# Optimization experiments

Hardware: AMD Instinct MI355X
Metric: run time of the kernel (lower is better)

The kernel has to match this reference:

```python
import jax, jax.numpy as jnp
import numpy as np

N = 100_000      # nodes
E = 1_600_000    # edges (avg degree 16)
F_IN = 128
H = 128
C = 10
G = 2000         # graphs
S = 200          # sets
MAX_SET = G // S # 10; uniform set sizes -> static max_set_size (see notes)


def _linear_init(key, fan_in, fan_out):
    s = 1.0 / np.sqrt(fan_in)
    kw, kb = jax.random.split(key)
    W = jax.random.uniform(kw, (fan_in, fan_out), minval=-s, maxval=s, dtype=jnp.float32)
    b = jax.random.uniform(kb, (fan_out,), minval=-s, maxval=s, dtype=jnp.float32)
    return W, b


def setup_inputs() -> dict:
    key = jax.random.key(0)
    ks = jax.random.split(key, 10)
    x = jax.random.normal(ks[0], (N, F_IN), dtype=jnp.float32)
    edge_index = jax.random.randint(ks[1], (2, E), 0, N, dtype=jnp.int32)
    batch = ((jnp.arange(N) * G) // N).astype(jnp.int32)          # sorted, 50 nodes/graph
    set_batch = (jnp.arange(G) % S).astype(jnp.int32)             # 10 graphs/set
    W1, b1 = _linear_init(ks[2], F_IN, H)
    W2, b2 = _linear_init(ks[3], H, H)
    W3, b3 = _linear_init(ks[4], H, H)
    psiW1, psib1 = _linear_init(ks[5], H, H)
    psiW2, psib2 = _linear_init(ks[6], H, H)
    phiW1, phib1 = _linear_init(ks[7], H, H)
    phiW2, phib2 = _linear_init(ks[8], H, C)
    return dict(x=x, edge_index=edge_index, batch=batch, set_batch=set_batch,
                W1=W1, b1=b1, W2=W2, b2=b2, W3=W3, b3=b3,
                psiW1=psiW1, psib1=psib1, psiW2=psiW2, psib2=psib2,
                phiW1=phiW1, phib1=phib1, phiW2=phiW2, phib2=phib2)


def _gcn_conv(x, src, dst, norm, W, b):
    # GCNConv: out = scatter_add(norm * (xW)[src] -> dst) + b
    h = x @ W
    msg = h[src] * norm[:, None]
    return jax.ops.segment_sum(msg, dst, num_segments=N) + b


def reference(x, edge_index, batch, set_batch,
              W1, b1, W2, b2, W3, b3,
              psiW1, psib1, psiW2, psib2, phiW1, phib1, phiW2, phib2):
    # add self loops, symmetric normalization D^-1/2 (A+I) D^-1/2
    loops = jnp.arange(N, dtype=edge_index.dtype)
    src = jnp.concatenate([edge_index[0], loops])
    dst = jnp.concatenate([edge_index[1], loops])
    deg = jax.ops.segment_sum(jnp.ones(src.shape, x.dtype), dst, num_segments=N)
    dinv = jnp.where(deg > 0, jax.lax.rsqrt(deg), 0.0)
    norm = dinv[src] * dinv[dst]

    h = jax.nn.relu(_gcn_conv(x, src, dst, norm, W1, b1))   # dropout is eval-mode identity
    h = jax.nn.relu(_gcn_conv(h, src, dst, norm, W2, b2))
    h = jax.nn.relu(_gcn_conv(h, src, dst, norm, W3, b3))

    # global mean pool over nodes -> [G, H]
    sums = jax.ops.segment_sum(h, batch, num_segments=G)
    cnts = jax.ops.segment_sum(jnp.ones((N,), h.dtype), batch, num_segments=G)
    graph_emb = sums / jnp.maximum(cnts, 1.0)[:, None]

    # ragged-to-padded pack: [S, MAX_SET, H]
    set_sizes = jax.ops.segment_sum(jnp.ones((G,), jnp.int32), set_batch, num_segments=S)
    offsets = jnp.concatenate([jnp.zeros((1,), jnp.int32), jnp.cumsum(set_sizes)])
    sorted_idx = jnp.argsort(set_batch)                      # stable by default
    positions_sorted = jnp.arange(G, dtype=jnp.int32) - offsets[set_batch[sorted_idx]]
    positions = jnp.zeros((G,), jnp.int32).at[sorted_idx].set(positions_sorted)
    x_pad = jnp.zeros((S, MAX_SET, H), x.dtype).at[set_batch, positions].set(graph_emb)

    # DeepSets: phi(sum_i psi(x_i))
    p = jnp.tanh(jax.nn.relu(x_pad @ psiW1 + psib1) @ psiW2 + psib2)
    agg = p.sum(axis=1)                                      # [S, H]
    return jax.nn.relu(agg @ phiW1 + phib1) @ phiW2 + phib2  # [S, C]
```

## Files before the change

### kernel.cpp

```cpp
#include <hip/hip_runtime.h>
#include <hip/hip_bf16.h>
#include <hip/hip_fp16.h>
#include <math.h>

#define NN 100000
#define EE 1600000
#define HH 128
#define GG 2000
#define SS 200
#define CC 10
#define NPG 50
#define PGS 10
#define NCLS 128
#define CLSW 782
#define EPB 4096
#define NBLKH 391
#define SCAN_N (NCLS * NBLKH)

typedef _Float16 f16x8 __attribute__((ext_vector_type(8)));
typedef float    f32x4 __attribute__((ext_vector_type(4)));


__global__ __launch_bounds__(256) void histo_kernel(const int* __restrict__ ei_dst,
                                                    int* __restrict__ blkcnt) {
    __shared__ int h[4][NCLS];
    for (int i = threadIdx.x; i < 4 * NCLS; i += 256) ((int*)h)[i] = 0;
    __syncthreads();
    int w = threadIdx.x >> 6;
    int base = blockIdx.x * EPB;
#pragma unroll
    for (int i = 0; i < 16; ++i) {
        int idx = base + i * 256 + threadIdx.x;
        if (idx < EE) {
            int d = __builtin_nontemporal_load(ei_dst + idx);
            atomicAdd(&h[w][(unsigned)d / CLSW], 1);
        }
    }
    __syncthreads();
    for (int c = threadIdx.x; c < NCLS; c += 256)
        blkcnt[c * NBLKH + blockIdx.x] = h[0][c] + h[1][c] + h[2][c] + h[3][c];
}

__global__ void scan_chunk_kernel(const int* __restrict__ v, int* __restrict__ outp,
                                  int* __restrict__ bsum, int n) {
    __shared__ int s[256];
    int tid = threadIdx.x;
    int i = blockIdx.x * 256 + tid;
    int x = (i < n) ? v[i] : 0;
    s[tid] = x;
    __syncthreads();
    for (int off = 1; off < 256; off <<= 1) {
        int y = (tid >= off) ? s[tid - off] : 0;
        __syncthreads();
        s[tid] += y;
        __syncthreads();
    }
    if (i < n) outp[i + 1] = s[tid];
    if (tid == 255) bsum[blockIdx.x] = s[255];
}

__global__ void scan_bsums_kernel(int* bsum, int nb) {
    __shared__ int s[512];
    int tid = threadIdx.x;
    int x = (tid < nb) ? bsum[tid] : 0;
    s[tid] = x;
    __syncthreads();
    for (int off = 1; off < 512; off <<= 1) {
        int y = (tid >= off) ? s[tid - off] : 0;
        __syncthreads();
        s[tid] += y;
        __syncthreads();
    }
    if (tid < nb) bsum[tid] = s[tid];
}

__global__ void scan_finish_kernel(int* __restrict__ outp, const int* __restrict__ bsum, int n) {
    int i = blockIdx.x * 256 + threadIdx.x;
    if (i < n) {
        if (blockIdx.x > 0) outp[i + 1] += bsum[blockIdx.x - 1];
    }
    if (i == 0) outp[0] = 0;
}

__global__ __launch_bounds__(256) void scatter_bin_kernel(const int* __restrict__ ei,
                                                          const int* __restrict__ blkoff,
                                                          long long* __restrict__ ebin) {
    __shared__ int cur[NCLS];
    for (int c = threadIdx.x; c < NCLS; c += 256) cur[c] = blkoff[c * NBLKH + blockIdx.x];
    __syncthreads();
    int base = blockIdx.x * EPB;
#pragma unroll
    for (int i = 0; i < 16; ++i) {
        int idx = base + i * 256 + threadIdx.x;
        if (idx < EE) {
            int s = __builtin_nontemporal_load(ei + idx);
            int d = __builtin_nontemporal_load(ei + EE + idx);
            int c = (unsigned)d / CLSW;
            int pos = atomicAdd(&cur[c], 1);
            ebin[pos] = ((long long)d << 32) | (unsigned)s;
        }
    }
}

__global__ __launch_bounds__(256) void count_dinv_kernel(const long long* __restrict__ ebin,
                                                         const int* __restrict__ blkoff,
                                                         int* __restrict__ degi,
                                                         float* __restrict__ dinv) {
    __shared__ int cnt[CLSW];
    int c = blockIdx.x;
    for (int i = threadIdx.x; i < CLSW; i += 256) cnt[i] = 0;
    __syncthreads();
    int beg = blkoff[c * NBLKH];
    int end = blkoff[(c + 1) * NBLKH];
    int n0 = c * CLSW;
    for (int k = beg + threadIdx.x; k < end; k += 256) {
        long long e = __builtin_nontemporal_load(ebin + k);
        atomicAdd(&cnt[(int)(e >> 32) - n0], 1);
    }
    __syncthreads();
    int nn = min(n0 + CLSW, NN) - n0;
    for (int i = threadIdx.x; i < nn; i += 256) {
        degi[n0 + i] = cnt[i];
        dinv[n0 + i] = 1.0f / sqrtf((float)(cnt[i] + 1));
    }
}

__global__ __launch_bounds__(256) void fill_class_kernel(const long long* __restrict__ ebin,
                                                         const int* __restrict__ blkoff,
                                                         const int* __restrict__ row_ptr,
                                                         int* __restrict__ col) {
    __shared__ int cur[CLSW];
    int c = blockIdx.x;
    int n0 = c * CLSW;
    int nn = min(n0 + CLSW, NN) - n0;
    for (int i = threadIdx.x; i < nn; i += 256) cur[i] = row_ptr[n0 + i];
    __syncthreads();
    int beg = blkoff[c * NBLKH];
    int end = blkoff[(c + 1) * NBLKH];
    for (int k = beg + threadIdx.x; k < end; k += 256) {
        long long e = __builtin_nontemporal_load(ebin + k);
        int s = (int)(e & 0xffffffffll);
        int d = (int)(e >> 32);
        int o = atomicAdd(&cur[d - n0], 1);
        col[o] = s;
    }
}


#define WTP 136

template <bool IN32>
__global__ __launch_bounds__(256) void gemm_mfma_kernel(const void* __restrict__ Xv,
                                                        const float* __restrict__ W,
                                                        const float* __restrict__ dinv,
                                                        _Float16* __restrict__ Y, int nrows) {
    __shared__ _Float16 Wt[128][WTP];
    __shared__ _Float16 Ob[128][WTP];
    int tid = threadIdx.x;
    int row0 = blockIdx.x * 128;

    const float4* W4 = (const float4*)W;
#pragma unroll
    for (int it = 0; it < 16; ++it) {
        int f = it * 256 + tid;
        int k = f >> 5;
        int c = (f & 31) << 2;
        float4 v = W4[f];
        Wt[c + 0][k] = (_Float16)v.x;
        Wt[c + 1][k] = (_Float16)v.y;
        Wt[c + 2][k] = (_Float16)v.z;
        Wt[c + 3][k] = (_Float16)v.w;
    }
    __syncthreads();

    int wave = tid >> 6;
    int l = tid & 63;
    int arow = l & 15;
    int kg = l >> 4;
    int baseRow = row0 + wave * 32;

    f16x8 afrag[2][4];
#pragma unroll
    for (int rt = 0; rt < 2; ++rt) {
        int r = baseRow + rt * 16 + arow;
        r = min(r, nrows - 1);
        if (IN32) {
            const float* xr = ((const float*)Xv) + (size_t)r * 128;
#pragma unroll
            for (int ks = 0; ks < 4; ++ks) {
                int k0 = ks * 32 + kg * 8;
                float4 a = ((const float4*)xr)[k0 >> 2];
                float4 b = ((const float4*)xr)[(k0 >> 2) + 1];
                f16x8 v;
                v[0] = (_Float16)a.x; v[1] = (_Float16)a.y;
                v[2] = (_Float16)a.z; v[3] = (_Float16)a.w;
                v[4] = (_Float16)b.x; v[5] = (_Float16)b.y;
                v[6] = (_Float16)b.z; v[7] = (_Float16)b.w;
                afrag[rt][ks] = v;
            }
        } else {
            const f16x8* xr = (const f16x8*)(((const _Float16*)Xv) + (size_t)r * 128);
#pragma unroll
            for (int ks = 0; ks < 4; ++ks) afrag[rt][ks] = xr[ks * 4 + kg];
        }
    }

    f32x4 acc[2][8];
#pragma unroll
    for (int rt = 0; rt < 2; ++rt)
#pragma unroll
        for (int ct = 0; ct < 8; ++ct) acc[rt][ct] = (f32x4){0.f, 0.f, 0.f, 0.f};

#pragma unroll
    for (int ct = 0; ct < 8; ++ct) {
#pragma unroll
        for (int ks = 0; ks < 4; ++ks) {
            f16x8 b = *(const f16x8*)&Wt[ct * 16 + arow][ks * 32 + kg * 8];
            acc[0][ct] = __builtin_amdgcn_mfma_f32_16x16x32_f16(afrag[0][ks], b, acc[0][ct], 0, 0, 0);
            acc[1][ct] = __builtin_amdgcn_mfma_f32_16x16x32_f16(afrag[1][ks], b, acc[1][ct], 0, 0, 0);
        }
    }

    float dv[2][4];
#pragma unroll
    for (int rt = 0; rt < 2; ++rt)
#pragma unroll
        for (int j = 0; j < 4; ++j) {
            int r = baseRow + rt * 16 + 4 * kg + j;
            dv[rt][j] = dinv[min(r, nrows - 1)];
        }

#pragma unroll
    for (int rt = 0; rt < 2; ++rt)
#pragma unroll
        for (int ct = 0; ct < 8; ++ct)
#pragma unroll
            for (int j = 0; j < 4; ++j)
                Ob[wave * 32 + rt * 16 + 4 * kg + j][ct * 16 + arow] =
                    (_Float16)(acc[rt][ct][j] * dv[rt][j]);

#pragma unroll
    for (int i = 0; i < 8; ++i) {
        int q = i * 64 + l;
        int lrow = q >> 4;
        int c = q & 15;
        int r = baseRow + lrow;
        if (r < nrows) {
            f16x8 v = *(const f16x8*)&Ob[wave * 32 + lrow][c * 8];
            *(f16x8*)(Y + (size_t)r * 128 + c * 8) = v;
        }
    }
}


__global__ __launch_bounds__(256) void aggregate_kernel(const __half* __restrict__ hw,
                                                        const int* __restrict__ rp,
                                                        const int* __restrict__ col,
                                                        const float* __restrict__ dinv,
                                                        const float* __restrict__ bias,
                                                        __half* __restrict__ outp, int n) {
    int wid = threadIdx.x >> 6;
    int lane = threadIdx.x & 63;
    int i = blockIdx.x * 4 + wid;
    if (i >= n) return;
    const __half2* hw2 = (const __half2*)hw;
    float2 a0, a1, a2, a3;
    {
        float2 self = __half22float2(hw2[(size_t)i * 64 + lane]);
        a0.x = self.x; a0.y = self.y;
    }
    a1 = make_float2(0.f, 0.f);
    a2 = make_float2(0.f, 0.f);
    a3 = make_float2(0.f, 0.f);
    int j0 = rp[i], j1 = rp[i + 1];
    int j = j0;
    for (; j + 8 <= j1; j += 8) {
        int s0 = col[j + 0];
        int s1 = col[j + 1];
        int s2 = col[j + 2];
        int s3 = col[j + 3];
        int s4 = col[j + 4];
        int s5 = col[j + 5];
        int s6 = col[j + 6];
        int s7 = col[j + 7];
        __half2 v0 = hw2[(size_t)s0 * 64 + lane];
        __half2 v1 = hw2[(size_t)s1 * 64 + lane];
        __half2 v2 = hw2[(size_t)s2 * 64 + lane];
        __half2 v3 = hw2[(size_t)s3 * 64 + lane];
        __half2 v4 = hw2[(size_t)s4 * 64 + lane];
        __half2 v5 = hw2[(size_t)s5 * 64 + lane];
        __half2 v6 = hw2[(size_t)s6 * 64 + lane];
        __half2 v7 = hw2[(size_t)s7 * 64 + lane];
        float2 f;
        f = __half22float2(v0); a0.x += f.x; a0.y += f.y;
        f = __half22float2(v1); a1.x += f.x; a1.y += f.y;
        f = __half22float2(v2); a2.x += f.x; a2.y += f.y;
        f = __half22float2(v3); a3.x += f.x; a3.y += f.y;
        f = __half22float2(v4); a0.x += f.x; a0.y += f.y;
        f = __half22float2(v5); a1.x += f.x; a1.y += f.y;
        f = __half22float2(v6); a2.x += f.x; a2.y += f.y;
        f = __half22float2(v7); a3.x += f.x; a3.y += f.y;
    }
    for (; j + 4 <= j1; j += 4) {
        int s0 = col[j + 0];
        int s1 = col[j + 1];
        int s2 = col[j + 2];
        int s3 = col[j + 3];
        __half2 v0 = hw2[(size_t)s0 * 64 + lane];
        __half2 v1 = hw2[(size_t)s1 * 64 + lane];
        __half2 v2 = hw2[(size_t)s2 * 64 + lane];
        __half2 v3 = hw2[(size_t)s3 * 64 + lane];
        float2 f;
        f = __half22float2(v0); a0.x += f.x; a0.y += f.y;
        f = __half22float2(v1); a1.x += f.x; a1.y += f.y;
        f = __half22float2(v2); a2.x += f.x; a2.y += f.y;
        f = __half22float2(v3); a3.x += f.x; a3.y += f.y;
    }
    for (; j < j1; ++j) {
        int s = col[j];
        float2 f = __half22float2(hw2[(size_t)s * 64 + lane]);
        a0.x += f.x; a0.y += f.y;
    }
    float di = dinv[i];
    float2 acc;
    acc.x = ((a0.x + a1.x) + (a2.x + a3.x)) * di;
    acc.y = ((a0.y + a1.y) + (a2.y + a3.y)) * di;
    float2 bv = ((const float2*)bias)[lane];
    float rx = fmaxf(acc.x + bv.x, 0.f);
    float ry = fmaxf(acc.y + bv.y, 0.f);
    ((__half2*)outp)[(size_t)i * 64 + lane] = __floats2half2_rn(rx, ry);
}


__global__ __launch_bounds__(256) void pool_kernel(const __half* __restrict__ h,
                                                   float* __restrict__ gemb) {
    int wid = threadIdx.x >> 6;
    int lane = threadIdx.x & 63;
    int g = blockIdx.x * 4 + wid;
    if (g >= GG) return;
    const __half2* h2 = (const __half2*)h;
    float2 acc = {0.f, 0.f};
    size_t base = (size_t)g * NPG * 64;
    for (int r = 0; r < NPG; ++r) {
        float2 v = __half22float2(h2[base + (size_t)r * 64 + lane]);
        acc.x += v.x;
        acc.y += v.y;
    }
    float2 o;
    o.x = acc.x / (float)NPG;
    o.y = acc.y / (float)NPG;
    ((float2*)gemb)[(size_t)g * 64 + lane] = o;
}


__global__ __launch_bounds__(128) void psi_kernel(const float* __restrict__ gemb,
                                                  const float* __restrict__ W1,
                                                  const float* __restrict__ b1,
                                                  const float* __restrict__ W2,
                                                  const float* __restrict__ b2,
                                                  float* __restrict__ pbuf) {
    __shared__ float e[128];
    __shared__ float t[128];
    int g = blockIdx.x;
    int c = threadIdx.x;
    e[c] = gemb[(size_t)g * 128 + c];
    __syncthreads();
    float acc = b1[c];
#pragma unroll 8
    for (int k = 0; k < 128; ++k) acc += e[k] * W1[k * 128 + c];
    t[c] = fmaxf(acc, 0.f);
    __syncthreads();
    float acc2 = b2[c];
#pragma unroll 8
    for (int k = 0; k < 128; ++k) acc2 += t[k] * W2[k * 128 + c];
    pbuf[(size_t)g * 128 + c] = tanhf(acc2);
}


__global__ __launch_bounds__(128) void phi_kernel(const float* __restrict__ pbuf,
                                                  const float* __restrict__ W1,
                                                  const float* __restrict__ b1,
                                                  const float* __restrict__ W2,
                                                  const float* __restrict__ b2,
                                                  float* __restrict__ out) {
    __shared__ float a[128];
    __shared__ float u[128];
    int s = blockIdx.x;
    int c = threadIdx.x;
    float acc = 0.f;
#pragma unroll
    for (int p = 0; p < PGS; ++p) acc += pbuf[(size_t)(s + p * SS) * 128 + c];
    a[c] = acc;
    __syncthreads();
    float acc1 = b1[c];
#pragma unroll 8
    for (int k = 0; k < 128; ++k) acc1 += a[k] * W1[k * 128 + c];
    u[c] = fmaxf(acc1, 0.f);
    __syncthreads();
    if (c < CC) {
        float acc2 = b2[c];
#pragma unroll 8
        for (int k = 0; k < 128; ++k) acc2 += u[k] * W2[k * CC + c];
        out[(size_t)s * CC + c] = acc2;
    }
}


extern "C" void kernel_launch(void* const* d_in, const int* in_sizes, int n_in,
                              void* d_out, int out_size, void* d_ws, size_t ws_size,
                              hipStream_t stream) {
    const float* x   = (const float*)d_in[0];
    const int* ei    = (const int*)d_in[1];
    const float* W1  = (const float*)d_in[4];
    const float* b1  = (const float*)d_in[5];
    const float* W2  = (const float*)d_in[6];
    const float* b2  = (const float*)d_in[7];
    const float* W3  = (const float*)d_in[8];
    const float* b3  = (const float*)d_in[9];
    const float* pW1 = (const float*)d_in[10];
    const float* pb1 = (const float*)d_in[11];
    const float* pW2 = (const float*)d_in[12];
    const float* pb2 = (const float*)d_in[13];
    const float* fW1 = (const float*)d_in[14];
    const float* fb1 = (const float*)d_in[15];
    const float* fW2 = (const float*)d_in[16];
    const float* fb2 = (const float*)d_in[17];
    float* out = (float*)d_out;

    char* p = (char*)d_ws;
    auto alloc = [&](size_t bytes) {
        char* r = p;
        p += (bytes + 255) & ~(size_t)255;
        return r;
    };
    int*       degi    = (int*)alloc((size_t)NN * 4);
    float*     dinv    = (float*)alloc((size_t)NN * 4);
    int*       row_ptr = (int*)alloc((size_t)(NN + 1) * 4);
    int*       bsum    = (int*)alloc(512 * 4);
    int*       bsum2   = (int*)alloc(512 * 4);
    int*       blkcnt  = (int*)alloc((size_t)SCAN_N * 4);
    int*       blkoff  = (int*)alloc((size_t)(SCAN_N + 1) * 4);
    int*       col     = (int*)alloc((size_t)EE * 4);
    long long* ebin    = (long long*)alloc((size_t)EE * 8);
    _Float16*  bufA    = (_Float16*)alloc((size_t)NN * HH * 2);
    __half*    bufB    = (__half*)alloc((size_t)NN * HH * 2);
    float*     gemb    = (float*)alloc((size_t)GG * HH * 4);
    float*     pbuf    = (float*)alloc((size_t)GG * HH * 4);

    const int nblkN = (NN + 255) / 256;
    const int nblkS = (SCAN_N + 255) / 256;

    histo_kernel<<<NBLKH, 256, 0, stream>>>(ei + EE, blkcnt);
    scan_chunk_kernel<<<nblkS, 256, 0, stream>>>(blkcnt, blkoff, bsum2, SCAN_N);
    scan_bsums_kernel<<<1, 512, 0, stream>>>(bsum2, nblkS);
    scan_finish_kernel<<<nblkS, 256, 0, stream>>>(blkoff, bsum2, SCAN_N);
    scatter_bin_kernel<<<NBLKH, 256, 0, stream>>>(ei, blkoff, ebin);
    count_dinv_kernel<<<NCLS, 256, 0, stream>>>(ebin, blkoff, degi, dinv);
    scan_chunk_kernel<<<nblkN, 256, 0, stream>>>(degi, row_ptr, bsum, NN);
    scan_bsums_kernel<<<1, 512, 0, stream>>>(bsum, nblkN);
    scan_finish_kernel<<<nblkN, 256, 0, stream>>>(row_ptr, bsum, NN);
    fill_class_kernel<<<NCLS, 256, 0, stream>>>(ebin, blkoff, row_ptr, col);

    const int gemmBlocks = (NN + 127) / 128;
    const int aggBlocks  = (NN + 3) / 4;

    gemm_mfma_kernel<true><<<gemmBlocks, 256, 0, stream>>>(x, W1, dinv, bufA, NN);
    aggregate_kernel<<<aggBlocks, 256, 0, stream>>>((const __half*)bufA, row_ptr, col, dinv, b1, bufB, NN);
    gemm_mfma_kernel<false><<<gemmBlocks, 256, 0, stream>>>(bufB, W2, dinv, bufA, NN);
    aggregate_kernel<<<aggBlocks, 256, 0, stream>>>((const __half*)bufA, row_ptr, col, dinv, b2, bufB, NN);
    gemm_mfma_kernel<false><<<gemmBlocks, 256, 0, stream>>>(bufB, W3, dinv, bufA, NN);
    aggregate_kernel<<<aggBlocks, 256, 0, stream>>>((const __half*)bufA, row_ptr, col, dinv, b3, bufB, NN);

    pool_kernel<<<(GG + 3) / 4, 256, 0, stream>>>(bufB, gemb);
    psi_kernel<<<GG, 128, 0, stream>>>(gemb, pW1, pb1, pW2, pb2, pbuf);
    phi_kernel<<<SS, 128, 0, stream>>>(pbuf, fW1, fb1, fW2, fb2, out);
}
```

Before: 380.6 us.

## Fuse row_ptr scan into degree count and split aggregation across half-waves

```diff
diff --git a/kernel.cpp b/kernel.cpp
--- a/kernel.cpp
+++ b/kernel.cpp
@@ -104,9 +104,10 @@
 
 __global__ __launch_bounds__(256) void count_dinv_kernel(const long long* __restrict__ ebin,
                                                          const int* __restrict__ blkoff,
-                                                         int* __restrict__ degi,
+                                                         int* __restrict__ row_ptr,
                                                          float* __restrict__ dinv) {
     __shared__ int cnt[CLSW];
+    __shared__ int part[256];
     int c = blockIdx.x;
     for (int i = threadIdx.x; i < CLSW; i += 256) cnt[i] = 0;
     __syncthreads();
@@ -119,10 +120,35 @@
     }
     __syncthreads();
     int nn = min(n0 + CLSW, NN) - n0;
-    for (int i = threadIdx.x; i < nn; i += 256) {
-        degi[n0 + i] = cnt[i];
-        dinv[n0 + i] = 1.0f / sqrtf((float)(cnt[i] + 1));
-    }
+    int t = threadIdx.x;
+    int base = t * 4;
+    int lpre[4];
+    int lsum = 0;
+#pragma unroll
+    for (int i = 0; i < 4; ++i) {
+        int idx = base + i;
+        int v = (idx < nn) ? cnt[idx] : 0;
+        lpre[i] = lsum;
+        lsum += v;
+    }
+    part[t] = lsum;
+    __syncthreads();
+    for (int off = 1; off < 256; off <<= 1) {
+        int y = (t >= off) ? part[t - off] : 0;
+        __syncthreads();
+        part[t] += y;
+        __syncthreads();
+    }
+    int add = beg + ((t > 0) ? part[t - 1] : 0);
+#pragma unroll
+    for (int i = 0; i < 4; ++i) {
+        int idx = base + i;
+        if (idx < nn) {
+            row_ptr[n0 + idx] = add + lpre[i];
+            dinv[n0 + idx] = 1.0f / sqrtf((float)(cnt[idx] + 1));
+        }
+    }
+    if (t == 0) row_ptr[n0 + nn] = end;
 }
 
 __global__ __launch_bounds__(256) void fill_class_kernel(const long long* __restrict__ ebin,
@@ -253,6 +279,14 @@
 }
 
 
+__device__ __forceinline__ void acc_h4(float4& a, float2 raw) {
+    __half2 lo = *(__half2*)&raw.x;
+    __half2 hi = *(__half2*)&raw.y;
+    float2 f0 = __half22float2(lo);
+    float2 f1 = __half22float2(hi);
+    a.x += f0.x; a.y += f0.y; a.z += f1.x; a.w += f1.y;
+}
+
 __global__ __launch_bounds__(256) void aggregate_kernel(const __half* __restrict__ hw,
                                                         const int* __restrict__ rp,
                                                         const int* __restrict__ col,
@@ -263,72 +297,66 @@
     int lane = threadIdx.x & 63;
     int i = blockIdx.x * 4 + wid;
     if (i >= n) return;
-    const __half2* hw2 = (const __half2*)hw;
-    float2 a0, a1, a2, a3;
-    {
-        float2 self = __half22float2(hw2[(size_t)i * 64 + lane]);
-        a0.x = self.x; a0.y = self.y;
-    }
-    a1 = make_float2(0.f, 0.f);
-    a2 = make_float2(0.f, 0.f);
-    a3 = make_float2(0.f, 0.f);
+    int sub = lane >> 5;
+    int q = lane & 31;
+    const float2* hw4 = (const float2*)hw;
+
+    float4 b0 = {0.f, 0.f, 0.f, 0.f};
+    float4 b1 = {0.f, 0.f, 0.f, 0.f};
+    float4 b2 = {0.f, 0.f, 0.f, 0.f};
+    float4 b3 = {0.f, 0.f, 0.f, 0.f};
+
+    if (sub == 0) acc_h4(b2, hw4[(size_t)i * 32 + q]);
+
     int j0 = rp[i], j1 = rp[i + 1];
+    int m = j1 - j0;
+    int pairs = m >> 1;
     int j = j0;
-    for (; j + 8 <= j1; j += 8) {
-        int s0 = col[j + 0];
-        int s1 = col[j + 1];
-        int s2 = col[j + 2];
-        int s3 = col[j + 3];
-        int s4 = col[j + 4];
-        int s5 = col[j + 5];
-        int s6 = col[j + 6];
-        int s7 = col[j + 7];
-        __half2 v0 = hw2[(size_t)s0 * 64 + lane];
-        __half2 v1 = hw2[(size_t)s1 * 64 + lane];
-        __half2 v2 = hw2[(size_t)s2 * 64 + lane];
-        __half2 v3 = hw2[(size_t)s3 * 64 + lane];
-        __half2 v4 = hw2[(size_t)s4 * 64 + lane];
-        __half2 v5 = hw2[(size_t)s5 * 64 + lane];
-        __half2 v6 = hw2[(size_t)s6 * 64 + lane];
-        __half2 v7 = hw2[(size_t)s7 * 64 + lane];
-        float2 f;
-        f = __half22float2(v0); a0.x += f.x; a0.y += f.y;
-        f = __half22float2(v1); a1.x += f.x; a1.y += f.y;
-        f = __half22float2(v2); a2.x += f.x; a2.y += f.y;
-        f = __half22float2(v3); a3.x += f.x; a3.y += f.y;
-        f = __half22float2(v4); a0.x += f.x; a0.y += f.y;
-        f = __half22float2(v5); a1.x += f.x; a1.y += f.y;
-        f = __half22float2(v6); a2.x += f.x; a2.y += f.y;
-        f = __half22float2(v7); a3.x += f.x; a3.y += f.y;
-    }
-    for (; j + 4 <= j1; j += 4) {
-        int s0 = col[j + 0];
-        int s1 = col[j + 1];
-        int s2 = col[j + 2];
-        int s3 = col[j + 3];
-        __half2 v0 = hw2[(size_t)s0 * 64 + lane];
-        __half2 v1 = hw2[(size_t)s1 * 64 + lane];
-        __half2 v2 = hw2[(size_t)s2 * 64 + lane];
-        __half2 v3 = hw2[(size_t)s3 * 64 + lane];
-        float2 f;
-        f = __half22float2(v0); a0.x += f.x; a0.y += f.y;
-        f = __half22float2(v1); a1.x += f.x; a1.y += f.y;
-        f = __half22float2(v2); a2.x += f.x; a2.y += f.y;
-        f = __half22float2(v3); a3.x += f.x; a3.y += f.y;
-    }
-    for (; j < j1; ++j) {
-        int s = col[j];
-        float2 f = __half22float2(hw2[(size_t)s * 64 + lane]);
-        a0.x += f.x; a0.y += f.y;
-    }
-    float di = dinv[i];
-    float2 acc;
-    acc.x = ((a0.x + a1.x) + (a2.x + a3.x)) * di;
-    acc.y = ((a0.y + a1.y) + (a2.y + a3.y)) * di;
-    float2 bv = ((const float2*)bias)[lane];
-    float rx = fmaxf(acc.x + bv.x, 0.f);
-    float ry = fmaxf(acc.y + bv.y, 0.f);
-    ((__half2*)outp)[(size_t)i * 64 + lane] = __floats2half2_rn(rx, ry);
+    for (; pairs >= 4; pairs -= 4, j += 8) {
+        int e0 = __builtin_nontemporal_load(col + j + 0 + sub);
+        int e1 = __builtin_nontemporal_load(col + j + 2 + sub);
+        int e2 = __builtin_nontemporal_load(col + j + 4 + sub);
+        int e3 = __builtin_nontemporal_load(col + j + 6 + sub);
+        float2 r0 = hw4[(size_t)e0 * 32 + q];
+        float2 r1 = hw4[(size_t)e1 * 32 + q];
+        float2 r2 = hw4[(size_t)e2 * 32 + q];
+        float2 r3 = hw4[(size_t)e3 * 32 + q];
+        acc_h4(b0, r0);
+        acc_h4(b1, r1);
+        acc_h4(b2, r2);
+        acc_h4(b3, r3);
+    }
+    for (; pairs > 0; --pairs, j += 2) {
+        int e = __builtin_nontemporal_load(col + j + sub);
+        acc_h4(b0, hw4[(size_t)e * 32 + q]);
+    }
+    if ((m & 1) && sub == 0) {
+        int e = __builtin_nontemporal_load(col + j1 - 1);
+        acc_h4(b1, hw4[(size_t)e * 32 + q]);
+    }
+
+    float4 acc;
+    acc.x = (b0.x + b1.x) + (b2.x + b3.x);
+    acc.y = (b0.y + b1.y) + (b2.y + b3.y);
+    acc.z = (b0.z + b1.z) + (b2.z + b3.z);
+    acc.w = (b0.w + b1.w) + (b2.w + b3.w);
+    acc.x += __shfl_xor(acc.x, 32);
+    acc.y += __shfl_xor(acc.y, 32);
+    acc.z += __shfl_xor(acc.z, 32);
+    acc.w += __shfl_xor(acc.w, 32);
+
+    if (sub == 0) {
+        float di = dinv[i];
+        float4 bv = ((const float4*)bias)[q];
+        float rx = fmaxf(acc.x * di + bv.x, 0.f);
+        float ry = fmaxf(acc.y * di + bv.y, 0.f);
+        float rz = fmaxf(acc.z * di + bv.z, 0.f);
+        float rw = fmaxf(acc.w * di + bv.w, 0.f);
+        float2 pk;
+        *(__half2*)&pk.x = __floats2half2_rn(rx, ry);
+        *(__half2*)&pk.y = __floats2half2_rn(rz, rw);
+        ((float2*)outp)[(size_t)i * 32 + q] = pk;
+    }
 }
 
 
@@ -433,10 +461,8 @@
         p += (bytes + 255) & ~(size_t)255;
         return r;
     };
-    int*       degi    = (int*)alloc((size_t)NN * 4);
     float*     dinv    = (float*)alloc((size_t)NN * 4);
     int*       row_ptr = (int*)alloc((size_t)(NN + 1) * 4);
-    int*       bsum    = (int*)alloc(512 * 4);
     int*       bsum2   = (int*)alloc(512 * 4);
     int*       blkcnt  = (int*)alloc((size_t)SCAN_N * 4);
     int*       blkoff  = (int*)alloc((size_t)(SCAN_N + 1) * 4);
@@ -447,7 +473,6 @@
     float*     gemb    = (float*)alloc((size_t)GG * HH * 4);
     float*     pbuf    = (float*)alloc((size_t)GG * HH * 4);
 
-    const int nblkN = (NN + 255) / 256;
     const int nblkS = (SCAN_N + 255) / 256;
 
     histo_kernel<<<NBLKH, 256, 0, stream>>>(ei + EE, blkcnt);
@@ -455,10 +480,7 @@
     scan_bsums_kernel<<<1, 512, 0, stream>>>(bsum2, nblkS);
     scan_finish_kernel<<<nblkS, 256, 0, stream>>>(blkoff, bsum2, SCAN_N);
     scatter_bin_kernel<<<NBLKH, 256, 0, stream>>>(ei, blkoff, ebin);
-    count_dinv_kernel<<<NCLS, 256, 0, stream>>>(ebin, blkoff, degi, dinv);
-    scan_chunk_kernel<<<nblkN, 256, 0, stream>>>(degi, row_ptr, bsum, NN);
-    scan_bsums_kernel<<<1, 512, 0, stream>>>(bsum, nblkN);
-    scan_finish_kernel<<<nblkN, 256, 0, stream>>>(row_ptr, bsum, NN);
+    count_dinv_kernel<<<NCLS, 256, 0, stream>>>(ebin, blkoff, row_ptr, dinv);
     fill_class_kernel<<<NCLS, 256, 0, stream>>>(ebin, blkoff, row_ptr, col);
 
     const int gemmBlocks = (NN + 127) / 128;
```

After: 417.6 us. 9.7% more time.

## Pack edge bins into 32-bit words and fuse row_ptr scan into count kernel

Applied to the files above, without the earlier changes.

```diff
diff --git a/kernel.cpp b/kernel.cpp
--- a/kernel.cpp
+++ b/kernel.cpp
@@ -21,6 +21,7 @@
 typedef float    f32x4 __attribute__((ext_vector_type(4)));
 
 
+
 __global__ __launch_bounds__(256) void histo_kernel(const int* __restrict__ ei_dst,
                                                     int* __restrict__ blkcnt) {
     __shared__ int h[4][NCLS];
@@ -84,7 +85,7 @@
 
 __global__ __launch_bounds__(256) void scatter_bin_kernel(const int* __restrict__ ei,
                                                           const int* __restrict__ blkoff,
-                                                          long long* __restrict__ ebin) {
+                                                          unsigned int* __restrict__ ebin) {
     __shared__ int cur[NCLS];
     for (int c = threadIdx.x; c < NCLS; c += 256) cur[c] = blkoff[c * NBLKH + blockIdx.x];
     __syncthreads();
@@ -97,16 +98,17 @@
             int d = __builtin_nontemporal_load(ei + EE + idx);
             int c = (unsigned)d / CLSW;
             int pos = atomicAdd(&cur[c], 1);
-            ebin[pos] = ((long long)d << 32) | (unsigned)s;
-        }
-    }
-}
-
-__global__ __launch_bounds__(256) void count_dinv_kernel(const long long* __restrict__ ebin,
+            ebin[pos] = ((unsigned)(d - c * CLSW) << 17) | (unsigned)s;
+        }
+    }
+}
+
+__global__ __launch_bounds__(256) void count_dinv_kernel(const unsigned int* __restrict__ ebin,
                                                          const int* __restrict__ blkoff,
-                                                         int* __restrict__ degi,
+                                                         int* __restrict__ row_ptr,
                                                          float* __restrict__ dinv) {
     __shared__ int cnt[CLSW];
+    __shared__ int part[256];
     int c = blockIdx.x;
     for (int i = threadIdx.x; i < CLSW; i += 256) cnt[i] = 0;
     __syncthreads();
@@ -114,18 +116,43 @@
     int end = blkoff[(c + 1) * NBLKH];
     int n0 = c * CLSW;
     for (int k = beg + threadIdx.x; k < end; k += 256) {
-        long long e = __builtin_nontemporal_load(ebin + k);
-        atomicAdd(&cnt[(int)(e >> 32) - n0], 1);
+        unsigned int e = __builtin_nontemporal_load(ebin + k);
+        atomicAdd(&cnt[e >> 17], 1);
     }
     __syncthreads();
     int nn = min(n0 + CLSW, NN) - n0;
-    for (int i = threadIdx.x; i < nn; i += 256) {
-        degi[n0 + i] = cnt[i];
-        dinv[n0 + i] = 1.0f / sqrtf((float)(cnt[i] + 1));
-    }
-}
-
-__global__ __launch_bounds__(256) void fill_class_kernel(const long long* __restrict__ ebin,
+    int t = threadIdx.x;
+    int base = t * 4;
+    int lpre[4];
+    int lsum = 0;
+#pragma unroll
+    for (int i = 0; i < 4; ++i) {
+        int idx = base + i;
+        int v = (idx < nn) ? cnt[idx] : 0;
+        lpre[i] = lsum;
+        lsum += v;
+    }
+    part[t] = lsum;
+    __syncthreads();
+    for (int off = 1; off < 256; off <<= 1) {
+        int y = (t >= off) ? part[t - off] : 0;
+        __syncthreads();
+        part[t] += y;
+        __syncthreads();
+    }
+    int add = beg + ((t > 0) ? part[t - 1] : 0);
+#pragma unroll
+    for (int i = 0; i < 4; ++i) {
+        int idx = base + i;
+        if (idx < nn) {
+            row_ptr[n0 + idx] = add + lpre[i];
+            dinv[n0 + idx] = 1.0f / sqrtf((float)(cnt[idx] + 1));
+        }
+    }
+    if (t == 0) row_ptr[n0 + nn] = end;
+}
+
+__global__ __launch_bounds__(256) void fill_class_kernel(const unsigned int* __restrict__ ebin,
                                                          const int* __restrict__ blkoff,
                                                          const int* __restrict__ row_ptr,
                                                          int* __restrict__ col) {
@@ -138,11 +165,9 @@
     int beg = blkoff[c * NBLKH];
     int end = blkoff[(c + 1) * NBLKH];
     for (int k = beg + threadIdx.x; k < end; k += 256) {
-        long long e = __builtin_nontemporal_load(ebin + k);
-        int s = (int)(e & 0xffffffffll);
-        int d = (int)(e >> 32);
-        int o = atomicAdd(&cur[d - n0], 1);
-        col[o] = s;
+        unsigned int e = __builtin_nontemporal_load(ebin + k);
+        int o = atomicAdd(&cur[e >> 17], 1);
+        col[o] = (int)(e & 0x1FFFFu);
     }
 }
 
@@ -433,21 +458,18 @@
         p += (bytes + 255) & ~(size_t)255;
         return r;
     };
-    int*       degi    = (int*)alloc((size_t)NN * 4);
-    float*     dinv    = (float*)alloc((size_t)NN * 4);
-    int*       row_ptr = (int*)alloc((size_t)(NN + 1) * 4);
-    int*       bsum    = (int*)alloc(512 * 4);
-    int*       bsum2   = (int*)alloc(512 * 4);
-    int*       blkcnt  = (int*)alloc((size_t)SCAN_N * 4);
-    int*       blkoff  = (int*)alloc((size_t)(SCAN_N + 1) * 4);
-    int*       col     = (int*)alloc((size_t)EE * 4);
-    long long* ebin    = (long long*)alloc((size_t)EE * 8);
-    _Float16*  bufA    = (_Float16*)alloc((size_t)NN * HH * 2);
-    __half*    bufB    = (__half*)alloc((size_t)NN * HH * 2);
-    float*     gemb    = (float*)alloc((size_t)GG * HH * 4);
-    float*     pbuf    = (float*)alloc((size_t)GG * HH * 4);
-
-    const int nblkN = (NN + 255) / 256;
+    float*        dinv    = (float*)alloc((size_t)NN * 4);
+    int*          row_ptr = (int*)alloc((size_t)(NN + 1) * 4);
+    int*          bsum2   = (int*)alloc(512 * 4);
+    int*          blkcnt  = (int*)alloc((size_t)SCAN_N * 4);
+    int*          blkoff  = (int*)alloc((size_t)(SCAN_N + 1) * 4);
+    int*          col     = (int*)alloc((size_t)EE * 4);
+    unsigned int* ebin    = (unsigned int*)alloc((size_t)EE * 4);
+    _Float16*     bufA    = (_Float16*)alloc((size_t)NN * HH * 2);
+    __half*       bufB    = (__half*)alloc((size_t)NN * HH * 2);
+    float*        gemb    = (float*)alloc((size_t)GG * HH * 4);
+    float*        pbuf    = (float*)alloc((size_t)GG * HH * 4);
+
     const int nblkS = (SCAN_N + 255) / 256;
 
     histo_kernel<<<NBLKH, 256, 0, stream>>>(ei + EE, blkcnt);
@@ -455,10 +477,7 @@
     scan_bsums_kernel<<<1, 512, 0, stream>>>(bsum2, nblkS);
     scan_finish_kernel<<<nblkS, 256, 0, stream>>>(blkoff, bsum2, SCAN_N);
     scatter_bin_kernel<<<NBLKH, 256, 0, stream>>>(ei, blkoff, ebin);
-    count_dinv_kernel<<<NCLS, 256, 0, stream>>>(ebin, blkoff, degi, dinv);
-    scan_chunk_kernel<<<nblkN, 256, 0, stream>>>(degi, row_ptr, bsum, NN);
-    scan_bsums_kernel<<<1, 512, 0, stream>>>(bsum, nblkN);
-    scan_finish_kernel<<<nblkN, 256, 0, stream>>>(row_ptr, bsum, NN);
+    count_dinv_kernel<<<NCLS, 256, 0, stream>>>(ebin, blkoff, row_ptr, dinv);
     fill_class_kernel<<<NCLS, 256, 0, stream>>>(ebin, blkoff, row_ptr, col);
 
     const int gemmBlocks = (NN + 127) / 128;
```

Measured after the change: 374.9 us. Within noise of the previous version (-1.5%).
